# Optimization experiments

Hardware: AMD Instinct MI355X
Metric: run time of the kernel (lower is better)

The kernel has to match this reference:

```python
import jax, jax.numpy as jnp
import numpy as np


def setup_inputs() -> dict:
    key = jax.random.key(0)
    k1, k2 = jax.random.split(key)
    B, H, W = 32, 512, 512
    H_SHAPE = (3, 3)  # filter shape -> w has h0*h1 - 1 = 8 taps
    x = jax.random.normal(k1, (B, H, W, 1), dtype=jnp.float32)
    w = jax.random.uniform(k2, (1, H_SHAPE[0] * H_SHAPE[1] - 1), dtype=jnp.float32)
    return {"x": x, "w": w}


def reference(x, w):
    # x: [B, H, W, 1] float32, w: [1, h0*h1-1] float32
    B, H, W = x.shape[0], x.shape[1], x.shape[2]
    xm = x.reshape(-1, H, W)  # [B, H, W]

    # Zero-pad the filter taps to the full [H, W] grid (top-left placement).
    hm1 = jnp.pad(w, ((0, H - w.shape[0]), (0, W - w.shape[1])))

    cplx = jnp.complex64
    # Inverse filter spectrum and its three flipped/rolled (frequency-reversed) copies.
    gm1f = 1.0 / jnp.fft.fft2(hm1.astype(cplx))                 # [H, W]
    gm2f = jnp.roll(jnp.flip(gm1f, axis=0), shift=1, axis=0)
    gm3f = jnp.roll(jnp.flip(gm1f, axis=1), shift=1, axis=1)
    gm4f = jnp.roll(jnp.flip(gm3f, axis=0), shift=1, axis=0)
    gmf = (gm1f * gm2f) * (gm3f * gm4f)                         # [H, W]

    # Apply combined inverse filter in the frequency domain.
    ymf = gmf * jnp.fft.fft2(xm.astype(cplx))                   # [B, H, W]
    ym = jnp.real(jnp.fft.ifft2(ymf)).astype(jnp.float32)       # tf.cast complex->float takes real part
    return ym.reshape(-1, H, W, 1)
```

## Files before the change

kernel.cpp:

```cpp
#include <hip/hip_runtime.h>


#define WDIM 512
#define PAIRS_PER_BLOCK 4

struct cplx { float re, im; };
__device__ __forceinline__ cplx cadd(cplx a, cplx b) { return {a.re + b.re, a.im + b.im}; }
__device__ __forceinline__ cplx csub(cplx a, cplx b) { return {a.re - b.re, a.im - b.im}; }
__device__ __forceinline__ cplx cmul(cplx a, cplx b) {
    return {a.re * b.re - a.im * b.im, a.re * b.im + a.im * b.re};
}
template <int SIGN> __device__ __forceinline__ cplx cmul_i(cplx a) {
    return (SIGN > 0) ? cplx{-a.im, a.re} : cplx{a.im, -a.re};
}

template <int SIGN> __device__ __forceinline__ cplx wroot512(int k) {
    float f = (float)k * (1.0f / 512.0f);
    float sn = __builtin_amdgcn_sinf(f);
    float cs = __builtin_amdgcn_cosf(f);
    return {cs, SIGN > 0 ? sn : -sn};
}

template <int SIGN> __device__ __forceinline__ void dft8(const cplx* a, cplx* b) {
    cplx t0 = cadd(a[0], a[4]), t4 = csub(a[0], a[4]);
    cplx t1 = cadd(a[1], a[5]), t5 = csub(a[1], a[5]);
    cplx t2 = cadd(a[2], a[6]), t6 = cmul_i<SIGN>(csub(a[2], a[6]));
    cplx t3 = cadd(a[3], a[7]), t7 = cmul_i<SIGN>(csub(a[3], a[7]));
    cplx E0 = cadd(t0, t2), E2 = csub(t0, t2);
    cplx E1 = cadd(t4, t6), E3 = csub(t4, t6);
    cplx O0 = cadd(t1, t3), O2 = csub(t1, t3);
    cplx O1 = cadd(t5, t7), O3 = csub(t5, t7);
    const float C = 0.70710678118654752f;
    cplx w1 = {C, SIGN * C};
    cplx w3 = {-C, SIGN * C};
    cplx O1w = cmul(O1, w1);
    cplx O2w = cmul_i<SIGN>(O2);
    cplx O3w = cmul(O3, w3);
    b[0] = cadd(E0, O0);  b[4] = csub(E0, O0);
    b[1] = cadd(E1, O1w); b[5] = csub(E1, O1w);
    b[2] = cadd(E2, O2w); b[6] = csub(E2, O2w);
    b[3] = cadd(E3, O3w); b[7] = csub(E3, O3w);
}

template <int SIGN> __device__ __forceinline__ void twiddle8(cplx* b, int k512) {
#pragma unroll
    for (int t = 1; t < 8; ++t) {
        cplx w = wroot512<SIGN>((k512 * t) & 511);
        b[t] = cmul(b[t], w);
    }
}

__device__ __forceinline__ int phi(int q) { return q + ((q >> 6) << 2); }

__global__ __launch_bounds__(256, 4) void fft_conv_kernel(const float* __restrict__ x,
                                                          const float* __restrict__ w,
                                                          float* __restrict__ y) {
    __shared__ float lds[PAIRS_PER_BLOCK][2][544];
    const int wv = threadIdx.x >> 6;
    const int u = threadIdx.x & 63;
    const int pair = blockIdx.x * PAIRS_PER_BLOCK + wv;
    float* lre = lds[wv][0];
    float* lim = lds[wv][1];
    const float* x1 = x + (size_t)(2 * pair) * WDIM;
    const float* x2 = x1 + WDIM;

    cplx a[8], b[8];
#pragma unroll
    for (int j = 0; j < 8; ++j) {
        int idx = u + 64 * j;
        a[j].re = x1[idx];
        a[j].im = x2[idx];
    }

    float Gv[8];
    {
        const int c = ((u & 7) << 3) + (u >> 3);
        cplx m[8], Hv[8];
        m[0] = {w[0], 0.0f};
#pragma unroll
        for (int j = 1; j < 8; ++j) {
            cplx e = wroot512<-1>((c * j) & 511);
            float wj = w[j];
            m[j].re = wj * e.re;
            m[j].im = wj * e.im;
        }
        dft8<-1>(m, Hv);
#pragma unroll
        for (int t = 0; t < 8; ++t) {
            float m2 = Hv[t].re * Hv[t].re + Hv[t].im * Hv[t].im;
            Gv[t] = 1.0f / (m2 * m2);
        }
    }

    dft8<-1>(a, b);
    twiddle8<-1>(b, u);
#pragma unroll
    for (int t = 0; t < 8; ++t) {
        int p = phi(u + 64 * t);
        lre[p] = b[t].re; lim[p] = b[t].im;
    }
    __syncthreads();

    {
        const int base = ((u >> 3) << 6) + (u & 7);
#pragma unroll
        for (int j = 0; j < 8; ++j) {
            int p = phi(base + 8 * j);
            a[j].re = lre[p]; a[j].im = lim[p];
        }
        dft8<-1>(a, b);
        twiddle8<-1>(b, 8 * (u & 7));
#pragma unroll
        for (int t = 0; t < 8; ++t) {
            int p = phi(base + 8 * t);
            lre[p] = b[t].re; lim[p] = b[t].im;
        }
    }
    __syncthreads();

    {
        const int base = 8 * u;
#pragma unroll
        for (int j = 0; j < 8; ++j) {
            int p = phi(base + j);
            a[j].re = lre[p]; a[j].im = lim[p];
        }
        dft8<-1>(a, b);
#pragma unroll
        for (int t = 0; t < 8; ++t) {
            b[t].re *= Gv[t]; b[t].im *= Gv[t];
        }
        dft8<+1>(b, a);
#pragma unroll
        for (int j = 0; j < 8; ++j) {
            int p = phi(base + j);
            lre[p] = a[j].re; lim[p] = a[j].im;
        }
    }
    __syncthreads();

    {
        const int base = ((u >> 3) << 6) + (u & 7);
#pragma unroll
        for (int t = 0; t < 8; ++t) {
            int p = phi(base + 8 * t);
            a[t].re = lre[p]; a[t].im = lim[p];
        }
        twiddle8<+1>(a, 8 * (u & 7));
        dft8<+1>(a, b);
#pragma unroll
        for (int j = 0; j < 8; ++j) {
            int p = phi(base + 8 * j);
            lre[p] = b[j].re; lim[p] = b[j].im;
        }
    }
    __syncthreads();

    {
#pragma unroll
        for (int t = 0; t < 8; ++t) {
            int p = phi(u + 64 * t);
            a[t].re = lre[p]; a[t].im = lim[p];
        }
        twiddle8<+1>(a, u);
        dft8<+1>(a, b);
        const float s = 1.0f / 512.0f;
        float* y1 = y + (size_t)(2 * pair) * WDIM;
        float* y2 = y1 + WDIM;
#pragma unroll
        for (int j = 0; j < 8; ++j) {
            int idx = u + 64 * j;
            y1[idx] = b[j].re * s;
            y2[idx] = b[j].im * s;
        }
    }
}

extern "C" void kernel_launch(void* const* d_in, const int* in_sizes, int n_in,
                              void* d_out, int out_size, void* d_ws, size_t ws_size,
                              hipStream_t stream) {
    const float* x = (const float*)d_in[0];
    const float* w = (const float*)d_in[1];
    float* y = (float*)d_out;

    fft_conv_kernel<<<dim3(16384 / (2 * PAIRS_PER_BLOCK)), dim3(256), 0, stream>>>(x, w, y);
}
```

Measured before the change: 88.36 us.

## Precompute inverse filter spectrum in separate kernel and use single-wave blocks

Moves the per-thread computation of the combined inverse filter gain into a tiny prologue kernel that writes 512 scaled gains to workspace, folding the 1/512 normalization in. The main kernel now loads its gains and runs one 64-thread wavefront per block with its own LDS buffer. It alternates two LDS padding schemes around extra barriers, and drops the modulo masking on twiddle angles since the hardware sin/cos take revolutions. This trades redundant per-wave trig and DFT work for an extra launch, a global load and additional barriers.

```diff
diff --git a/kernel.cpp b/kernel.cpp
--- a/kernel.cpp
+++ b/kernel.cpp
@@ -2,7 +2,6 @@
 
 
 #define WDIM 512
-#define PAIRS_PER_BLOCK 4
 
 struct cplx { float re, im; };
 __device__ __forceinline__ cplx cadd(cplx a, cplx b) { return {a.re + b.re, a.im + b.im}; }
@@ -45,22 +44,37 @@
 template <int SIGN> __device__ __forceinline__ void twiddle8(cplx* b, int k512) {
 #pragma unroll
     for (int t = 1; t < 8; ++t) {
-        cplx w = wroot512<SIGN>((k512 * t) & 511);
+        cplx w = wroot512<SIGN>(k512 * t);
         b[t] = cmul(b[t], w);
     }
 }
 
-__device__ __forceinline__ int phi(int q) { return q + ((q >> 6) << 2); }
+__device__ __forceinline__ int phiA(int q) { return q + ((q >> 6) << 2); }
+__device__ __forceinline__ int phiB(int q) { return q + ((q >> 6) << 1); }
 
-__global__ __launch_bounds__(256, 4) void fft_conv_kernel(const float* __restrict__ x,
-                                                          const float* __restrict__ w,
-                                                          float* __restrict__ y) {
-    __shared__ float lds[PAIRS_PER_BLOCK][2][544];
-    const int wv = threadIdx.x >> 6;
-    const int u = threadIdx.x & 63;
-    const int pair = blockIdx.x * PAIRS_PER_BLOCK + wv;
-    float* lre = lds[wv][0];
-    float* lim = lds[wv][1];
+__global__ __launch_bounds__(512) void build_gdr_kernel(const float* __restrict__ w,
+                                                        float* __restrict__ Gdr) {
+    const int p = threadIdx.x;
+    const int k = ((p & 7) << 6) | (p & 56) | (p >> 6);
+    float hr = 0.f, hi = 0.f;
+#pragma unroll
+    for (int j = 0; j < 8; ++j) {
+        float f = (float)((k * j) & 511) * (1.0f / 512.0f);
+        float wj = w[j];
+        hr += wj * __builtin_amdgcn_cosf(f);
+        hi -= wj * __builtin_amdgcn_sinf(f);
+    }
+    float m2 = hr * hr + hi * hi;
+    Gdr[p] = (1.0f / 512.0f) / (m2 * m2);
+}
+
+__global__ __launch_bounds__(64, 4) void fft_conv_kernel(const float* __restrict__ x,
+                                                         const float* __restrict__ Gdr,
+                                                         float* __restrict__ y) {
+    __shared__ float lre[544];
+    __shared__ float lim[544];
+    const int u = threadIdx.x;
+    const int pair = blockIdx.x;
     const float* x1 = x + (size_t)(2 * pair) * WDIM;
     const float* x2 = x1 + WDIM;
 
@@ -73,30 +87,14 @@
     }
 
     float Gv[8];
-    {
-        const int c = ((u & 7) << 3) + (u >> 3);
-        cplx m[8], Hv[8];
-        m[0] = {w[0], 0.0f};
 #pragma unroll
-        for (int j = 1; j < 8; ++j) {
-            cplx e = wroot512<-1>((c * j) & 511);
-            float wj = w[j];
-            m[j].re = wj * e.re;
-            m[j].im = wj * e.im;
-        }
-        dft8<-1>(m, Hv);
-#pragma unroll
-        for (int t = 0; t < 8; ++t) {
-            float m2 = Hv[t].re * Hv[t].re + Hv[t].im * Hv[t].im;
-            Gv[t] = 1.0f / (m2 * m2);
-        }
-    }
+    for (int t = 0; t < 8; ++t) Gv[t] = Gdr[8 * u + t];
 
     dft8<-1>(a, b);
     twiddle8<-1>(b, u);
 #pragma unroll
     for (int t = 0; t < 8; ++t) {
-        int p = phi(u + 64 * t);
+        int p = phiA(u + 64 * t);
         lre[p] = b[t].re; lim[p] = b[t].im;
     }
     __syncthreads();
@@ -105,14 +103,15 @@
         const int base = ((u >> 3) << 6) + (u & 7);
 #pragma unroll
         for (int j = 0; j < 8; ++j) {
-            int p = phi(base + 8 * j);
+            int p = phiA(base + 8 * j);
             a[j].re = lre[p]; a[j].im = lim[p];
         }
         dft8<-1>(a, b);
         twiddle8<-1>(b, 8 * (u & 7));
+        __syncthreads();
 #pragma unroll
         for (int t = 0; t < 8; ++t) {
-            int p = phi(base + 8 * t);
+            int p = phiB(base + 8 * t);
             lre[p] = b[t].re; lim[p] = b[t].im;
         }
     }
@@ -122,7 +121,7 @@
         const int base = 8 * u;
 #pragma unroll
         for (int j = 0; j < 8; ++j) {
-            int p = phi(base + j);
+            int p = phiB(base + j);
             a[j].re = lre[p]; a[j].im = lim[p];
         }
         dft8<-1>(a, b);
@@ -133,7 +132,7 @@
         dft8<+1>(b, a);
 #pragma unroll
         for (int j = 0; j < 8; ++j) {
-            int p = phi(base + j);
+            int p = phiB(base + j);
             lre[p] = a[j].re; lim[p] = a[j].im;
         }
     }
@@ -143,14 +142,15 @@
         const int base = ((u >> 3) << 6) + (u & 7);
 #pragma unroll
         for (int t = 0; t < 8; ++t) {
-            int p = phi(base + 8 * t);
+            int p = phiB(base + 8 * t);
             a[t].re = lre[p]; a[t].im = lim[p];
         }
         twiddle8<+1>(a, 8 * (u & 7));
         dft8<+1>(a, b);
+        __syncthreads();
 #pragma unroll
         for (int j = 0; j < 8; ++j) {
-            int p = phi(base + 8 * j);
+            int p = phiA(base + 8 * j);
             lre[p] = b[j].re; lim[p] = b[j].im;
         }
     }
@@ -159,19 +159,18 @@
     {
 #pragma unroll
         for (int t = 0; t < 8; ++t) {
-            int p = phi(u + 64 * t);
+            int p = phiA(u + 64 * t);
             a[t].re = lre[p]; a[t].im = lim[p];
         }
         twiddle8<+1>(a, u);
         dft8<+1>(a, b);
-        const float s = 1.0f / 512.0f;
         float* y1 = y + (size_t)(2 * pair) * WDIM;
         float* y2 = y1 + WDIM;
 #pragma unroll
         for (int j = 0; j < 8; ++j) {
             int idx = u + 64 * j;
-            y1[idx] = b[j].re * s;
-            y2[idx] = b[j].im * s;
+            y1[idx] = b[j].re;
+            y2[idx] = b[j].im;
         }
     }
 }
@@ -182,6 +181,8 @@
     const float* x = (const float*)d_in[0];
     const float* w = (const float*)d_in[1];
     float* y = (float*)d_out;
+    float* Gdr = (float*)d_ws;
 
-    fft_conv_kernel<<<dim3(16384 / (2 * PAIRS_PER_BLOCK)), dim3(256), 0, stream>>>(x, w, y);
+    build_gdr_kernel<<<dim3(1), dim3(512), 0, stream>>>(w, Gdr);
+    fft_conv_kernel<<<dim3(8192), dim3(64), 0, stream>>>(x, Gdr, y);
 }
```

Measured after the change: 87.06 us. Within noise of the previous version (-1.5%).
